# Optimization experiments

Hardware: AMD Instinct MI355X
Metric: run time of the kernel (lower is better)

## Reference

```python
import jax, jax.numpy as jnp
import numpy as np

HID = 16
EMB = 32


def _cell_step(W_f, b_f, W_i, b_i, W_C, b_C, W_o, b_o):
    def step(carry, w):
        h, C = carry  # [B,H] each
        comb = jnp.concatenate([w, h], axis=1)  # [B, EMB+HID]
        f = jax.nn.sigmoid(comb @ W_f.T + b_f)
        i = jax.nn.sigmoid(comb @ W_i.T + b_i)
        C_t = jnp.tanh(comb @ W_C.T + b_C)
        C_new = f * C + i * C_t
        o = jax.nn.sigmoid(comb @ W_o.T + b_o)
        h_new = o * jnp.tanh(C_new)
        return (h_new, C_new), h_new
    return step


def setup_inputs() -> dict:
    key = jax.random.key(0)
    ks = jax.random.split(key, 16)
    V, S, B = 50257, 64, 32
    stdv = 1.0 / np.sqrt(HID)
    u = lambda k, shape: jax.random.uniform(k, shape, jnp.float32, -stdv, stdv)
    return {
        "input_batch": jax.random.randint(ks[0], (S, B), 0, V),
        "embedding": jax.random.normal(ks[1], (V, EMB), jnp.float32),
        "W_f": u(ks[2], (HID, EMB + HID)), "b_f": u(ks[3], (HID,)),
        "W_i": u(ks[4], (HID, EMB + HID)), "b_i": u(ks[5], (HID,)),
        "W_C": u(ks[6], (HID, EMB + HID)), "b_C": u(ks[7], (HID,)),
        "W_o": u(ks[8], (HID, EMB + HID)), "b_o": u(ks[9], (HID,)),
        "W_ho": u(ks[10], (V, 2 * HID)), "b_ho": u(ks[11], (V,)),
        "initial_hidden": u(ks[12], (1, HID)),
        "initial_C": u(ks[13], (1, HID)),
    }


def reference(input_batch, embedding, W_f, b_f, W_i, b_i, W_C, b_C, W_o, b_o,
              W_ho, b_ho, initial_hidden, initial_C):
    S, B = input_batch.shape
    emb = embedding[input_batch]  # [S,B,EMB]
    h0 = jnp.broadcast_to(initial_hidden, (B, HID))
    C0 = jnp.broadcast_to(initial_C, (B, HID))
    step = _cell_step(W_f, b_f, W_i, b_i, W_C, b_C, W_o, b_o)

    # Left-to-right: hLR[t] = hidden after consuming inputs[0..t-1]; hLR[0]=h0
    _, hL_out = jax.lax.scan(step, (h0, C0), emb)
    lefts = jnp.concatenate([h0[None], hL_out[:-1]], axis=0)  # hLR[i], i=0..S-1

    # Right-to-left over reversed sequence (shared cell weights, same init)
    _, r_out = jax.lax.scan(step, (h0, C0), emb[::-1])
    flipped = r_out[::-1]  # flipped[m] = hidden after consuming input[m]
    # prediction i uses hRL[i+2]: output after consuming input[i+1] (init for i=S-1)
    rights = jnp.concatenate([flipped[1:], h0[None]], axis=0)

    concat_h = jnp.concatenate([lefts, rights], axis=-1)  # [S,B,2H]
    logits = jnp.einsum('sbh,vh->sbv', concat_h, W_ho) + b_ho
    return jax.nn.log_softmax(logits, axis=-1)
```

## Files before the change

### kernel.cpp

```cpp
#include <hip/hip_runtime.h>
#include <hip/hip_bf16.h>
#include <math.h>

constexpr int S   = 64;
constexpr int B   = 32;
constexpr int HID = 16;
constexpr int EMB = 32;
constexpr int V   = 50257;
constexpr int CH  = 2*HID;
constexpr int IN  = EMB + HID;
constexpr int VPAD = 50272;
constexpr int NT   = VPAD/16;
constexpr int MT   = (S*B)/16;
constexpr int NSTRIP = 16;
constexpr int NT_PER = (NT + NSTRIP - 1)/NSTRIP;

typedef __attribute__((ext_vector_type(8))) short bf16x8;
typedef __attribute__((ext_vector_type(4))) float f32x4;

__device__ inline float sigm(float x)      { return 1.f/(1.f + __expf(-x)); }
__device__ inline float tanh_fast(float x) { return 1.f - 2.f/(1.f + __expf(2.f*x)); }

__global__ __launch_bounds__(256) void k0_conv(
    const float* __restrict__ Who, const float* __restrict__ bho,
    __hip_bfloat16* __restrict__ WhoB, float* __restrict__ bhoP)
{
    int i = blockIdx.x*256 + threadIdx.x;
    if (i < VPAD*CH) {
        int r = i >> 5;
        WhoB[i] = __float2bfloat16((r < V) ? Who[i] : 0.f);
    }
    if (i < VPAD) bhoP[i] = (i < V) ? bho[i] : -30.f;
}

__global__ __launch_bounds__(64) void k1_xw(
    const int* __restrict__ tok, const float* __restrict__ embT,
    const float* __restrict__ Wf, const float* __restrict__ bf,
    const float* __restrict__ Wi, const float* __restrict__ bi,
    const float* __restrict__ Wc, const float* __restrict__ bc,
    const float* __restrict__ Wo, const float* __restrict__ bo,
    float* __restrict__ xw)
{
    int sb = blockIdx.x, t = threadIdx.x;
    __shared__ float e[EMB];
    if (t < EMB) e[t] = embT[(long)tok[sb]*EMB + t];
    __syncthreads();
    int g = t >> 4, h = t & 15;
    const float* W  = (g==0) ? Wf : (g==1) ? Wi : (g==2) ? Wc : Wo;
    const float* bv = (g==0) ? bf : (g==1) ? bi : (g==2) ? bc : bo;
    const float* wr = W + h*IN;
    float acc = bv[h];
    #pragma unroll
    for (int k = 0; k < EMB; ++k) acc += e[k]*wr[k];
    xw[sb*64 + t] = acc;
}

__global__ __launch_bounds__(64) void k2_scan(
    const float* __restrict__ xw,
    const float* __restrict__ Wf, const float* __restrict__ Wi,
    const float* __restrict__ Wc, const float* __restrict__ Wo,
    const float* __restrict__ h0, const float* __restrict__ C0,
    __hip_bfloat16* __restrict__ hcatB)
{
    int id  = blockIdx.x;
    int dir = id >> 5, b = id & 31;
    int lane = threadIdx.x;
    int g = lane >> 4, hh = lane & 15;
    const float* W = (g==0) ? Wf : (g==1) ? Wi : (g==2) ? Wc : Wo;
    float U[HID];
    #pragma unroll
    for (int k = 0; k < HID; ++k) U[k] = W[hh*IN + EMB + k];
    float h = h0[hh], C = C0[hh];
    for (int step = 0; step < S; ++step) {
        int s  = dir ? (S-1-step) : step;
        int sb = s*B + b;
        if (g == 0) hcatB[sb*CH + dir*HID + hh] = __float2bfloat16(h);
        float p = xw[sb*64 + lane];
        #pragma unroll
        for (int k = 0; k < HID; ++k) p += U[k]*__shfl(h, k, 64);
        float a = (g==2) ? tanh_fast(p) : sigm(p);
        float fg = __shfl(a,      hh, 64);
        float ig = __shfl(a, 16 + hh, 64);
        float cg = __shfl(a, 32 + hh, 64);
        float og = __shfl(a, 48 + hh, 64);
        C = fg*C + ig*cg;
        h = og*tanh_fast(C);
    }
}

__global__ __launch_bounds__(256) void kA(
    const __hip_bfloat16* __restrict__ hcatB, const __hip_bfloat16* __restrict__ WhoB,
    const float* __restrict__ bhoP, float* __restrict__ row_sums)
{
    int t = threadIdx.x, w = t >> 6, lane = t & 63;
    int col = lane & 15, quad = lane >> 4;
    int r0 = (blockIdx.y*4 + w)*16;
    int n0 = blockIdx.x*NT_PER;
    int n1 = (n0 + NT_PER < NT) ? n0 + NT_PER : NT;
    bf16x8 a = *(const bf16x8*)((const short*)hcatB + (r0+col)*CH + quad*8);
    float acc0=0.f, acc1=0.f, acc2=0.f, acc3=0.f;
    for (int nt = n0; nt < n1; ++nt) {
        int v0 = nt*16;
        bf16x8 bfr = *(const bf16x8*)((const short*)WhoB + (long)(v0+col)*CH + quad*8);
        float bv = bhoP[v0+col];
        f32x4 d = {0.f,0.f,0.f,0.f};
        d = __builtin_amdgcn_mfma_f32_16x16x32_bf16(a, bfr, d, 0, 0, 0);
        acc0 += __expf(d[0]+bv);
        acc1 += __expf(d[1]+bv);
        acc2 += __expf(d[2]+bv);
        acc3 += __expf(d[3]+bv);
    }
    #pragma unroll
    for (int off = 1; off < 16; off <<= 1) {
        acc0 += __shfl_xor(acc0, off);
        acc1 += __shfl_xor(acc1, off);
        acc2 += __shfl_xor(acc2, off);
        acc3 += __shfl_xor(acc3, off);
    }
    if (col == 0) {
        atomicAdd(&row_sums[r0 + quad*4 + 0], acc0);
        atomicAdd(&row_sums[r0 + quad*4 + 1], acc1);
        atomicAdd(&row_sums[r0 + quad*4 + 2], acc2);
        atomicAdd(&row_sums[r0 + quad*4 + 3], acc3);
    }
}

__global__ __launch_bounds__(256) void k3b_log(
    const float* __restrict__ sums, float* __restrict__ logz)
{
    int i = blockIdx.x*256 + threadIdx.x;
    if (i < S*B) logz[i] = logf(sums[i]);
}

__global__ __launch_bounds__(256) void kB(
    const __hip_bfloat16* __restrict__ hcatB, const __hip_bfloat16* __restrict__ WhoB,
    const float* __restrict__ bhoP, const float* __restrict__ logz,
    float* __restrict__ out)
{
    int t = threadIdx.x, w = t >> 6, lane = t & 63;
    int col = lane & 15, quad = lane >> 4;
    int r0 = (blockIdx.y*4 + w)*16;
    int n0 = blockIdx.x*NT_PER;
    int n1 = (n0 + NT_PER < NT) ? n0 + NT_PER : NT;
    bf16x8 a = *(const bf16x8*)((const short*)hcatB + (r0+col)*CH + quad*8);
    float lz0 = logz[r0 + quad*4 + 0];
    float lz1 = logz[r0 + quad*4 + 1];
    float lz2 = logz[r0 + quad*4 + 2];
    float lz3 = logz[r0 + quad*4 + 3];
    float* prow = out + (long)(r0 + quad*4)*V + col;
    for (int nt = n0; nt < n1; ++nt) {
        int v0 = nt*16;
        bf16x8 bfr = *(const bf16x8*)((const short*)WhoB + (long)(v0+col)*CH + quad*8);
        float bv = bhoP[v0+col];
        f32x4 d = {0.f,0.f,0.f,0.f};
        d = __builtin_amdgcn_mfma_f32_16x16x32_bf16(a, bfr, d, 0, 0, 0);
        if (v0 + col < V) {
            prow[0L*V + v0] = d[0] + bv - lz0;
            prow[1L*V + v0] = d[1] + bv - lz1;
            prow[2L*V + v0] = d[2] + bv - lz2;
            prow[3L*V + v0] = d[3] + bv - lz3;
        }
    }
}

extern "C" void kernel_launch(void* const* d_in, const int* in_sizes, int n_in,
                              void* d_out, int out_size, void* d_ws, size_t ws_size,
                              hipStream_t stream)
{
    const int*   tok = (const int*)d_in[0];
    const float* emb = (const float*)d_in[1];
    const float* Wf  = (const float*)d_in[2];
    const float* bf  = (const float*)d_in[3];
    const float* Wi  = (const float*)d_in[4];
    const float* bi  = (const float*)d_in[5];
    const float* Wc  = (const float*)d_in[6];
    const float* bc  = (const float*)d_in[7];
    const float* Wo  = (const float*)d_in[8];
    const float* bo  = (const float*)d_in[9];
    const float* Who = (const float*)d_in[10];
    const float* bho = (const float*)d_in[11];
    const float* h0  = (const float*)d_in[12];
    const float* C0  = (const float*)d_in[13];
    float* out = (float*)d_out;

    char* p = (char*)d_ws;
    __hip_bfloat16* WhoB  = (__hip_bfloat16*)p; p += (size_t)VPAD*CH*2;
    __hip_bfloat16* hcatB = (__hip_bfloat16*)p; p += (size_t)S*B*CH*2;
    float* bhoP     = (float*)p; p += (size_t)VPAD*4;
    float* xw       = (float*)p; p += (size_t)S*B*64*4;
    float* row_sums = (float*)p; p += (size_t)S*B*4;
    float* logz     = (float*)p;

    hipMemsetAsync(row_sums, 0, S*B*sizeof(float), stream);
    k0_conv<<<dim3((VPAD*CH + 255)/256), dim3(256), 0, stream>>>(Who, bho, WhoB, bhoP);
    k1_xw<<<dim3(S*B), dim3(64), 0, stream>>>(tok, emb, Wf, bf, Wi, bi, Wc, bc, Wo, bo, xw);
    k2_scan<<<dim3(64), dim3(64), 0, stream>>>(xw, Wf, Wi, Wc, Wo, h0, C0, hcatB);
    dim3 g(NSTRIP, MT/4);
    kA<<<g, dim3(256), 0, stream>>>(hcatB, WhoB, bhoP, row_sums);
    k3b_log<<<dim3((S*B + 255)/256), dim3(256), 0, stream>>>(row_sums, logz);
    kB<<<g, dim3(256), 0, stream>>>(hcatB, WhoB, bhoP, logz, out);
}
```

Measured before the change: 625.0 us.

## Switch logits GEMMs to 32x32 MFMA, fuse prep kernels, drop log kernel

Merges the weight conversion, embedding projection and row_sums zeroing into one prep launch, which removes the memset and a launch. The logsumexp and output kernels move from 16x16x32 to 32x32x16 bf16 MFMA, fold bias and logz into the accumulator init, and compute logf inline, so the separate log kernel goes away. The strip count also doubles. The scan prefetches the next xw value and splits the recurrent dot product into four partial sums to shorten the dependency chain. The risks are higher register pressure from the 16-float accumulators and a different output store pattern.

```diff
diff --git a/kernel.cpp b/kernel.cpp
--- a/kernel.cpp
+++ b/kernel.cpp
@@ -10,49 +10,51 @@
 constexpr int CH  = 2*HID;
 constexpr int IN  = EMB + HID;
 constexpr int VPAD = 50272;
-constexpr int NT   = VPAD/16;
-constexpr int MT   = (S*B)/16;
-constexpr int NSTRIP = 16;
-constexpr int NT_PER = (NT + NSTRIP - 1)/NSTRIP;
-
-typedef __attribute__((ext_vector_type(8))) short bf16x8;
-typedef __attribute__((ext_vector_type(4))) float f32x4;
+constexpr int NT32 = VPAD/32;
+constexpr int MT32 = (S*B)/32;
+constexpr int NSTRIP = 32;
+constexpr int NT_PER = (NT32 + NSTRIP - 1)/NSTRIP;
+constexpr int NB_CONV = (VPAD*CH)/256;
+constexpr int NB_XW   = (S*B)/4;
+
+typedef __attribute__((ext_vector_type(8)))  short bf16x8;
+typedef __attribute__((ext_vector_type(16))) float f32x16;
 
 __device__ inline float sigm(float x)      { return 1.f/(1.f + __expf(-x)); }
 __device__ inline float tanh_fast(float x) { return 1.f - 2.f/(1.f + __expf(2.f*x)); }
 
-__global__ __launch_bounds__(256) void k0_conv(
-    const float* __restrict__ Who, const float* __restrict__ bho,
-    __hip_bfloat16* __restrict__ WhoB, float* __restrict__ bhoP)
-{
-    int i = blockIdx.x*256 + threadIdx.x;
-    if (i < VPAD*CH) {
-        int r = i >> 5;
-        WhoB[i] = __float2bfloat16((r < V) ? Who[i] : 0.f);
-    }
-    if (i < VPAD) bhoP[i] = (i < V) ? bho[i] : -30.f;
-}
-
-__global__ __launch_bounds__(64) void k1_xw(
-    const int* __restrict__ tok, const float* __restrict__ embT,
+__global__ __launch_bounds__(256) void kprep(
+    const int* __restrict__ tok, const float* __restrict__ emb,
     const float* __restrict__ Wf, const float* __restrict__ bf,
     const float* __restrict__ Wi, const float* __restrict__ bi,
     const float* __restrict__ Wc, const float* __restrict__ bc,
     const float* __restrict__ Wo, const float* __restrict__ bo,
-    float* __restrict__ xw)
-{
-    int sb = blockIdx.x, t = threadIdx.x;
-    __shared__ float e[EMB];
-    if (t < EMB) e[t] = embT[(long)tok[sb]*EMB + t];
-    __syncthreads();
-    int g = t >> 4, h = t & 15;
-    const float* W  = (g==0) ? Wf : (g==1) ? Wi : (g==2) ? Wc : Wo;
-    const float* bv = (g==0) ? bf : (g==1) ? bi : (g==2) ? bc : bo;
-    const float* wr = W + h*IN;
-    float acc = bv[h];
-    #pragma unroll
-    for (int k = 0; k < EMB; ++k) acc += e[k]*wr[k];
-    xw[sb*64 + t] = acc;
+    const float* __restrict__ Who, const float* __restrict__ bho,
+    __hip_bfloat16* __restrict__ WhoB, float* __restrict__ bhoP,
+    float* __restrict__ xw, float* __restrict__ row_sums)
+{
+    int bid = blockIdx.x, t = threadIdx.x;
+    if (bid < NB_CONV) {
+        int i = bid*256 + t;
+        int r = i >> 5;
+        WhoB[i] = __float2bfloat16((r < V) ? Who[i] : 0.f);
+        if (i < VPAD) bhoP[i] = (i < V) ? bho[i] : -30.f;
+        if (i < S*B)  row_sums[i] = 0.f;
+    } else {
+        int grp = t >> 6, lane = t & 63;
+        int sb  = (bid - NB_CONV)*4 + grp;
+        __shared__ float e[4][EMB];
+        if (lane < EMB) e[grp][lane] = emb[(long)tok[sb]*EMB + lane];
+        __syncthreads();
+        int g = lane >> 4, h = lane & 15;
+        const float* W  = (g==0) ? Wf : (g==1) ? Wi : (g==2) ? Wc : Wo;
+        const float* bv = (g==0) ? bf : (g==1) ? bi : (g==2) ? bc : bo;
+        const float* wr = W + h*IN;
+        float acc = bv[h];
+        #pragma unroll
+        for (int k = 0; k < EMB; ++k) acc += e[grp][k]*wr[k];
+        xw[sb*64 + lane] = acc;
+    }
 }
 
 __global__ __launch_bounds__(64) void k2_scan(
@@ -71,13 +73,22 @@
     #pragma unroll
     for (int k = 0; k < HID; ++k) U[k] = W[hh*IN + EMB + k];
     float h = h0[hh], C = C0[hh];
+    int sb     = dir ? (S-1)*B + b : b;
+    int stride = dir ? -B : B;
+    float xn = xw[sb*64 + lane];
     for (int step = 0; step < S; ++step) {
-        int s  = dir ? (S-1-step) : step;
-        int sb = s*B + b;
+        float p = xn;
+        if (step + 1 < S) xn = xw[(sb + stride)*64 + lane];
         if (g == 0) hcatB[sb*CH + dir*HID + hh] = __float2bfloat16(h);
-        float p = xw[sb*64 + lane];
-        #pragma unroll
-        for (int k = 0; k < HID; ++k) p += U[k]*__shfl(h, k, 64);
+        float q0 = 0.f, q1 = 0.f, q2 = 0.f, q3 = 0.f;
+        #pragma unroll
+        for (int k = 0; k < HID; k += 4) {
+            q0 += U[k  ]*__shfl(h, k,   64);
+            q1 += U[k+1]*__shfl(h, k+1, 64);
+            q2 += U[k+2]*__shfl(h, k+2, 64);
+            q3 += U[k+3]*__shfl(h, k+3, 64);
+        }
+        p += (q0+q1) + (q2+q3);
         float a = (g==2) ? tanh_fast(p) : sigm(p);
         float fg = __shfl(a,      hh, 64);
         float ig = __shfl(a, 16 + hh, 64);
@@ -85,6 +96,7 @@
         float og = __shfl(a, 48 + hh, 64);
         C = fg*C + ig*cg;
         h = og*tanh_fast(C);
+        sb += stride;
     }
 }
 
@@ -93,72 +105,77 @@
     const float* __restrict__ bhoP, float* __restrict__ row_sums)
 {
     int t = threadIdx.x, w = t >> 6, lane = t & 63;
-    int col = lane & 15, quad = lane >> 4;
-    int r0 = (blockIdx.y*4 + w)*16;
+    int l31 = lane & 31, half = lane >> 5;
+    int r0 = (blockIdx.y*4 + w)*32;
     int n0 = blockIdx.x*NT_PER;
-    int n1 = (n0 + NT_PER < NT) ? n0 + NT_PER : NT;
-    bf16x8 a = *(const bf16x8*)((const short*)hcatB + (r0+col)*CH + quad*8);
-    float acc0=0.f, acc1=0.f, acc2=0.f, acc3=0.f;
+    int n1 = (n0 + NT_PER < NT32) ? n0 + NT_PER : NT32;
+    const short* hp = (const short*)hcatB + (r0 + l31)*CH + half*8;
+    bf16x8 a0 = *(const bf16x8*)hp;
+    bf16x8 a1 = *(const bf16x8*)(hp + 16);
+    float acc[16];
+    #pragma unroll
+    for (int r = 0; r < 16; ++r) acc[r] = 0.f;
     for (int nt = n0; nt < n1; ++nt) {
-        int v0 = nt*16;
-        bf16x8 bfr = *(const bf16x8*)((const short*)WhoB + (long)(v0+col)*CH + quad*8);
-        float bv = bhoP[v0+col];
-        f32x4 d = {0.f,0.f,0.f,0.f};
-        d = __builtin_amdgcn_mfma_f32_16x16x32_bf16(a, bfr, d, 0, 0, 0);
-        acc0 += __expf(d[0]+bv);
-        acc1 += __expf(d[1]+bv);
-        acc2 += __expf(d[2]+bv);
-        acc3 += __expf(d[3]+bv);
-    }
-    #pragma unroll
-    for (int off = 1; off < 16; off <<= 1) {
-        acc0 += __shfl_xor(acc0, off);
-        acc1 += __shfl_xor(acc1, off);
-        acc2 += __shfl_xor(acc2, off);
-        acc3 += __shfl_xor(acc3, off);
-    }
-    if (col == 0) {
-        atomicAdd(&row_sums[r0 + quad*4 + 0], acc0);
-        atomicAdd(&row_sums[r0 + quad*4 + 1], acc1);
-        atomicAdd(&row_sums[r0 + quad*4 + 2], acc2);
-        atomicAdd(&row_sums[r0 + quad*4 + 3], acc3);
-    }
-}
-
-__global__ __launch_bounds__(256) void k3b_log(
-    const float* __restrict__ sums, float* __restrict__ logz)
-{
-    int i = blockIdx.x*256 + threadIdx.x;
-    if (i < S*B) logz[i] = logf(sums[i]);
+        int v0 = nt*32;
+        const short* bp = (const short*)WhoB + (long)(v0 + l31)*CH + half*8;
+        bf16x8 b0 = *(const bf16x8*)bp;
+        bf16x8 b1 = *(const bf16x8*)(bp + 16);
+        float bv = bhoP[v0 + l31];
+        f32x16 d;
+        #pragma unroll
+        for (int r = 0; r < 16; ++r) d[r] = bv;
+        d = __builtin_amdgcn_mfma_f32_32x32x16_bf16(a0, b0, d, 0, 0, 0);
+        d = __builtin_amdgcn_mfma_f32_32x32x16_bf16(a1, b1, d, 0, 0, 0);
+        #pragma unroll
+        for (int r = 0; r < 16; ++r) acc[r] += __expf(d[r]);
+    }
+    #pragma unroll
+    for (int off = 1; off < 32; off <<= 1) {
+        #pragma unroll
+        for (int r = 0; r < 16; ++r) acc[r] += __shfl_xor(acc[r], off);
+    }
+    if (l31 == 0) {
+        #pragma unroll
+        for (int r = 0; r < 16; ++r)
+            atomicAdd(&row_sums[r0 + (r&3) + 8*(r>>2) + 4*half], acc[r]);
+    }
 }
 
 __global__ __launch_bounds__(256) void kB(
     const __hip_bfloat16* __restrict__ hcatB, const __hip_bfloat16* __restrict__ WhoB,
-    const float* __restrict__ bhoP, const float* __restrict__ logz,
+    const float* __restrict__ bhoP, const float* __restrict__ row_sums,
     float* __restrict__ out)
 {
     int t = threadIdx.x, w = t >> 6, lane = t & 63;
-    int col = lane & 15, quad = lane >> 4;
-    int r0 = (blockIdx.y*4 + w)*16;
+    int l31 = lane & 31, half = lane >> 5;
+    int r0 = (blockIdx.y*4 + w)*32;
     int n0 = blockIdx.x*NT_PER;
-    int n1 = (n0 + NT_PER < NT) ? n0 + NT_PER : NT;
-    bf16x8 a = *(const bf16x8*)((const short*)hcatB + (r0+col)*CH + quad*8);
-    float lz0 = logz[r0 + quad*4 + 0];
-    float lz1 = logz[r0 + quad*4 + 1];
-    float lz2 = logz[r0 + quad*4 + 2];
-    float lz3 = logz[r0 + quad*4 + 3];
-    float* prow = out + (long)(r0 + quad*4)*V + col;
+    int n1 = (n0 + NT_PER < NT32) ? n0 + NT_PER : NT32;
+    const short* hp = (const short*)hcatB + (r0 + l31)*CH + half*8;
+    bf16x8 a0 = *(const bf16x8*)hp;
+    bf16x8 a1 = *(const bf16x8*)(hp + 16);
+    float    lzr[16];
+    unsigned obase[16];
+    #pragma unroll
+    for (int r = 0; r < 16; ++r) {
+        int row = r0 + (r&3) + 8*(r>>2) + 4*half;
+        lzr[r]   = logf(row_sums[row]);
+        obase[r] = (unsigned)row*V + l31;
+    }
     for (int nt = n0; nt < n1; ++nt) {
-        int v0 = nt*16;
-        bf16x8 bfr = *(const bf16x8*)((const short*)WhoB + (long)(v0+col)*CH + quad*8);
-        float bv = bhoP[v0+col];
-        f32x4 d = {0.f,0.f,0.f,0.f};
-        d = __builtin_amdgcn_mfma_f32_16x16x32_bf16(a, bfr, d, 0, 0, 0);
-        if (v0 + col < V) {
-            prow[0L*V + v0] = d[0] + bv - lz0;
-            prow[1L*V + v0] = d[1] + bv - lz1;
-            prow[2L*V + v0] = d[2] + bv - lz2;
-            prow[3L*V + v0] = d[3] + bv - lz3;
+        int v0 = nt*32;
+        const short* bp = (const short*)WhoB + (long)(v0 + l31)*CH + half*8;
+        bf16x8 b0 = *(const bf16x8*)bp;
+        bf16x8 b1 = *(const bf16x8*)(bp + 16);
+        float bv = bhoP[v0 + l31];
+        f32x16 d;
+        #pragma unroll
+        for (int r = 0; r < 16; ++r) d[r] = bv - lzr[r];
+        d = __builtin_amdgcn_mfma_f32_32x32x16_bf16(a0, b0, d, 0, 0, 0);
+        d = __builtin_amdgcn_mfma_f32_32x32x16_bf16(a1, b1, d, 0, 0, 0);
+        if (v0 + l31 < V) {
+            #pragma unroll
+            for (int r = 0; r < 16; ++r) out[obase[r] + v0] = d[r];
         }
     }
 }
@@ -188,15 +205,13 @@
     __hip_bfloat16* hcatB = (__hip_bfloat16*)p; p += (size_t)S*B*CH*2;
     float* bhoP     = (float*)p; p += (size_t)VPAD*4;
     float* xw       = (float*)p; p += (size_t)S*B*64*4;
-    float* row_sums = (float*)p; p += (size_t)S*B*4;
-    float* logz     = (float*)p;
-
-    hipMemsetAsync(row_sums, 0, S*B*sizeof(float), stream);
-    k0_conv<<<dim3((VPAD*CH + 255)/256), dim3(256), 0, stream>>>(Who, bho, WhoB, bhoP);
-    k1_xw<<<dim3(S*B), dim3(64), 0, stream>>>(tok, emb, Wf, bf, Wi, bi, Wc, bc, Wo, bo, xw);
+    float* row_sums = (float*)p;
+
+    kprep<<<dim3(NB_CONV + NB_XW), dim3(256), 0, stream>>>(
+        tok, emb, Wf, bf, Wi, bi, Wc, bc, Wo, bo, Who, bho,
+        WhoB, bhoP, xw, row_sums);
     k2_scan<<<dim3(64), dim3(64), 0, stream>>>(xw, Wf, Wi, Wc, Wo, h0, C0, hcatB);
-    dim3 g(NSTRIP, MT/4);
+    dim3 g(NSTRIP, MT32/4);
     kA<<<g, dim3(256), 0, stream>>>(hcatB, WhoB, bhoP, row_sums);
-    k3b_log<<<dim3((S*B + 255)/256), dim3(256), 0, stream>>>(row_sums, logz);
-    kB<<<g, dim3(256), 0, stream>>>(hcatB, WhoB, bhoP, logz, out);
-}
+    kB<<<g, dim3(256), 0, stream>>>(hcatB, WhoB, bhoP, row_sums, out);
+}
```

New measurement: 620.0 us. No clear change (-0.8%).
